# Optimization experiments

Hardware: AMD Instinct MI355X
Metric: run time of the kernel (lower is better)

Reference implementation:

```python
import jax, jax.numpy as jnp
import numpy as np

N_BINS = 15
B, S, V = 2048, 3, 32000

def setup_inputs() -> dict:
    key = jax.random.key(0)
    k1, k2 = jax.random.split(key)
    logits = jax.random.normal(k1, (B, S, V), dtype=jnp.float32)
    targets = jax.random.randint(k2, (B, 4), 0, V, dtype=jnp.int64)
    return {"logits": logits, "targets": targets}

def reference(logits, targets):
    # softmax over vocab, then per-position max confidence and argmax prediction
    probs = jax.nn.softmax(logits, axis=-1)            # [B,S,V]
    p3 = probs[:, :3, :]                               # [B,3,V]
    confidences3 = jnp.max(p3, axis=2)                 # [B,3]
    preds = jnp.argmax(p3, axis=2)                     # [B,3]
    confidences = jnp.prod(confidences3, axis=1)       # [B]
    temp_t = targets[:, 1:]                            # [B,3]
    accuracies = (preds == temp_t).astype(jnp.float32) # [B,3]
    # accuracies[in_bin].mean() over a [n,3] slice == mean of per-row means
    row_acc = jnp.mean(accuracies, axis=1)             # [B]

    boundaries = jnp.linspace(0.0, 1.0, N_BINS + 1)
    lowers, uppers = boundaries[:-1], boundaries[1:]
    # vectorized binning instead of the original per-bin python loop
    in_bin = (confidences[None, :] > lowers[:, None]) & (confidences[None, :] <= uppers[:, None])  # [15,B]
    in_bin_f = in_bin.astype(jnp.float32)
    count = jnp.sum(in_bin_f, axis=1)                  # [15]
    n = jnp.float32(confidences.shape[0])
    prop_in_bin = count / n
    safe_count = jnp.maximum(count, 1.0)
    avg_conf = jnp.sum(in_bin_f * confidences[None, :], axis=1) / safe_count
    avg_acc = jnp.sum(in_bin_f * row_acc[None, :], axis=1) / safe_count
    per_bin = jnp.where(count > 0, jnp.abs(avg_conf - avg_acc) * prop_in_bin, 0.0)
    ece = jnp.sum(per_bin).reshape(1)
    return ece
```

## Files before the change

kernel.cpp:

```cpp
#include <hip/hip_runtime.h>
#include <hip/hip_bf16.h>
#include <math.h>

#define VOCAB   32000
#define BATCH   2048
#define SEQ     3
#define ROWS    (BATCH * SEQ)
#define THREADS 320
#define CHUNK   5
#define NCHUNK  5
#define NBINS   15

__device__ __forceinline__ void combine(float& m, float& s, int& idx,
                                        float m2, float s2, int idx2) {
    if (m2 > m)      { s = s * __expf(m - m2) + s2; m = m2; idx = idx2; }
    else if (m2 < m) { s = s + s2 * __expf(m2 - m); }
    else             { s += s2; idx = (idx2 < idx) ? idx2 : idx; }
}

__global__ __launch_bounds__(THREADS) void row_softmax_stats(
        const float* __restrict__ logits,
        float* __restrict__ maxprob,
        int*   __restrict__ amax)
{
    const int row = blockIdx.x;
    const int t   = threadIdx.x;
    const float4* base = (const float4*)(logits + (size_t)row * VOCAB);

    float m = -INFINITY;
    float s0 = 0.f, s1 = 0.f, s2 = 0.f, s3 = 0.f;
    int   idx = 0;

    float4 cur[CHUNK], nxt[CHUNK];
    #pragma unroll
    for (int u = 0; u < CHUNK; ++u) cur[u] = base[t + THREADS * u];

    #pragma unroll
    for (int c = 0; c < NCHUNK; ++c) {
        if (c + 1 < NCHUNK) {
            #pragma unroll
            for (int u = 0; u < CHUNK; ++u)
                nxt[u] = base[t + THREADS * ((c + 1) * CHUNK + u)];
        }
        #pragma unroll
        for (int u = 0; u < CHUNK; ++u) {
            float4 v = cur[u];
            float lm = fmaxf(fmaxf(v.x, v.y), fmaxf(v.z, v.w));
            if (lm > m) {
                float sc = __expf(m - lm);
                s0 *= sc; s1 *= sc; s2 *= sc; s3 *= sc;
                m = lm;
                const int f4 = t + THREADS * (c * CHUNK + u);
                idx = f4 * 4 + ((v.x == lm) ? 0 : (v.y == lm) ? 1 : (v.z == lm) ? 2 : 3);
            }
            s0 += __expf(v.x - m);
            s1 += __expf(v.y - m);
            s2 += __expf(v.z - m);
            s3 += __expf(v.w - m);
        }
        #pragma unroll
        for (int u = 0; u < CHUNK; ++u) cur[u] = nxt[u];
    }

    float s = (s0 + s1) + (s2 + s3);

    for (int off = 32; off > 0; off >>= 1) {
        float m2 = __shfl_down(m, off);
        float sx = __shfl_down(s, off);
        int   i2 = __shfl_down(idx, off);
        combine(m, s, idx, m2, sx, i2);
    }

    __shared__ float sm[THREADS / 64], ss[THREADS / 64];
    __shared__ int   si[THREADS / 64];
    const int wave = t >> 6;
    if ((t & 63) == 0) { sm[wave] = m; ss[wave] = s; si[wave] = idx; }
    __syncthreads();
    if (t == 0) {
        for (int w = 1; w < THREADS / 64; ++w) combine(m, s, idx, sm[w], ss[w], si[w]);
        maxprob[row] = 1.0f / s;
        amax[row]    = idx;
    }
}

__global__ __launch_bounds__(1024) void ece_reduce(
        const float* __restrict__ maxprob,
        const int*   __restrict__ amax,
        const int*   __restrict__ targets,
        float*       __restrict__ out)
{
    const int t = threadIdx.x;

    float c_cnt[NBINS], c_conf[NBINS], c_acc[NBINS];
    #pragma unroll
    for (int i = 0; i < NBINS; ++i) { c_cnt[i] = 0.f; c_conf[i] = 0.f; c_acc[i] = 0.f; }

    #pragma unroll
    for (int r = 0; r < BATCH / 1024; ++r) {
        const int b = t + r * 1024;
        float p0 = maxprob[b * 3 + 0];
        float p1 = maxprob[b * 3 + 1];
        float p2 = maxprob[b * 3 + 2];
        float conf = (p0 * p1) * p2;

        float acc = 0.f;
        acc += (amax[b * 3 + 0] == targets[b * 4 + 1]) ? 1.f : 0.f;
        acc += (amax[b * 3 + 1] == targets[b * 4 + 2]) ? 1.f : 0.f;
        acc += (amax[b * 3 + 2] == targets[b * 4 + 3]) ? 1.f : 0.f;
        float row_acc = acc * (1.0f / 3.0f);

        #pragma unroll
        for (int i = 0; i < NBINS; ++i) {
            float lo = (float)i       * (1.0f / 15.0f);
            float up = (float)(i + 1) * (1.0f / 15.0f);
            bool in = (conf > lo) && (conf <= up);
            if (in) { c_cnt[i] += 1.f; c_conf[i] += conf; c_acc[i] += row_acc; }
        }
    }

    #pragma unroll
    for (int i = 0; i < NBINS; ++i) {
        for (int off = 32; off > 0; off >>= 1) {
            c_cnt[i]  += __shfl_down(c_cnt[i],  off);
            c_conf[i] += __shfl_down(c_conf[i], off);
            c_acc[i]  += __shfl_down(c_acc[i],  off);
        }
    }

    __shared__ float s_cnt[NBINS], s_conf[NBINS], s_acc[NBINS];
    if (t < NBINS) { s_cnt[t] = 0.f; s_conf[t] = 0.f; s_acc[t] = 0.f; }
    __syncthreads();
    if ((t & 63) == 0) {
        #pragma unroll
        for (int i = 0; i < NBINS; ++i) {
            atomicAdd(&s_cnt[i],  c_cnt[i]);
            atomicAdd(&s_conf[i], c_conf[i]);
            atomicAdd(&s_acc[i],  c_acc[i]);
        }
    }
    __syncthreads();
    if (t == 0) {
        float ece = 0.f;
        #pragma unroll
        for (int i = 0; i < NBINS; ++i) {
            float cnt = s_cnt[i];
            if (cnt > 0.f) {
                float prop     = cnt / (float)BATCH;
                float safe_cnt = fmaxf(cnt, 1.0f);
                float avg_conf = s_conf[i] / safe_cnt;
                float avg_acc  = s_acc[i]  / safe_cnt;
                ece += fabsf(avg_conf - avg_acc) * prop;
            }
        }
        out[0] = ece;
    }
}

extern "C" void kernel_launch(void* const* d_in, const int* in_sizes, int n_in,
                              void* d_out, int out_size, void* d_ws, size_t ws_size,
                              hipStream_t stream) {
    const float* logits  = (const float*)d_in[0];
    const int*   targets = (const int*)d_in[1];
    float*       out     = (float*)d_out;

    float* maxprob = (float*)d_ws;
    int*   amax    = (int*)((char*)d_ws + ROWS * sizeof(float));

    row_softmax_stats<<<ROWS, THREADS, 0, stream>>>(logits, maxprob, amax);
    ece_reduce<<<1, 1024, 0, stream>>>(maxprob, amax, targets, out);
}
```

Measured before the change: 156.1 us.

## Assign one wave per softmax row, drop block reduction, use nontemporal loads

The row-stats kernel now maps each 32000-wide row to a single 64-lane wave, with four rows per 256-thread block, instead of one 320-thread block per row. This removes the shared-memory cross-wave combine and the __syncthreads. Loads become nontemporal vector loads in a simple loop unrolled by 5, replacing the explicit double-buffered prefetch. Each lane now processes 125 float4s serially, which lengthens per-wave dependency chains and relies on occupancy rather than explicit prefetch to hide memory latency.

Measured after the change: 138.3 us. -11.4%, faster.

```diff
diff --git a/kernel.cpp b/kernel.cpp
--- a/kernel.cpp
+++ b/kernel.cpp
@@ -2,14 +2,16 @@
 #include <hip/hip_bf16.h>
 #include <math.h>
 
-#define VOCAB   32000
-#define BATCH   2048
-#define SEQ     3
-#define ROWS    (BATCH * SEQ)
-#define THREADS 320
-#define CHUNK   5
-#define NCHUNK  5
-#define NBINS   15
+#define VOCAB     32000
+#define BATCH     2048
+#define SEQ       3
+#define ROWS      (BATCH * SEQ)
+#define WPB       4
+#define BLOCKSZ   (WPB * 64)
+#define NF4       (VOCAB / 4 / 64)
+#define NBINS     15
+
+typedef float f32x4 __attribute__((ext_vector_type(4)));
 
 __device__ __forceinline__ void combine(float& m, float& s, int& idx,
                                         float m2, float s2, int idx2) {
@@ -18,48 +20,35 @@
     else             { s += s2; idx = (idx2 < idx) ? idx2 : idx; }
 }
 
-__global__ __launch_bounds__(THREADS) void row_softmax_stats(
+__global__ __launch_bounds__(BLOCKSZ) void row_softmax_stats(
         const float* __restrict__ logits,
         float* __restrict__ maxprob,
         int*   __restrict__ amax)
 {
-    const int row = blockIdx.x;
-    const int t   = threadIdx.x;
-    const float4* base = (const float4*)(logits + (size_t)row * VOCAB);
+    const int wave = threadIdx.x >> 6;
+    const int lane = threadIdx.x & 63;
+    const int row  = blockIdx.x * WPB + wave;
+    const f32x4* base = (const f32x4*)(logits + (size_t)row * VOCAB);
 
     float m = -INFINITY;
     float s0 = 0.f, s1 = 0.f, s2 = 0.f, s3 = 0.f;
     int   idx = 0;
 
-    float4 cur[CHUNK], nxt[CHUNK];
-    #pragma unroll
-    for (int u = 0; u < CHUNK; ++u) cur[u] = base[t + THREADS * u];
-
-    #pragma unroll
-    for (int c = 0; c < NCHUNK; ++c) {
-        if (c + 1 < NCHUNK) {
-            #pragma unroll
-            for (int u = 0; u < CHUNK; ++u)
-                nxt[u] = base[t + THREADS * ((c + 1) * CHUNK + u)];
+    #pragma unroll 5
+    for (int i = 0; i < NF4; ++i) {
+        const int f4 = lane + 64 * i;
+        f32x4 v = __builtin_nontemporal_load(base + f4);
+        float lm = fmaxf(fmaxf(v.x, v.y), fmaxf(v.z, v.w));
+        if (lm > m) {
+            float sc = __expf(m - lm);
+            s0 *= sc; s1 *= sc; s2 *= sc; s3 *= sc;
+            m = lm;
+            idx = f4 * 4 + ((v.x == lm) ? 0 : (v.y == lm) ? 1 : (v.z == lm) ? 2 : 3);
         }
-        #pragma unroll
-        for (int u = 0; u < CHUNK; ++u) {
-            float4 v = cur[u];
-            float lm = fmaxf(fmaxf(v.x, v.y), fmaxf(v.z, v.w));
-            if (lm > m) {
-                float sc = __expf(m - lm);
-                s0 *= sc; s1 *= sc; s2 *= sc; s3 *= sc;
-                m = lm;
-                const int f4 = t + THREADS * (c * CHUNK + u);
-                idx = f4 * 4 + ((v.x == lm) ? 0 : (v.y == lm) ? 1 : (v.z == lm) ? 2 : 3);
-            }
-            s0 += __expf(v.x - m);
-            s1 += __expf(v.y - m);
-            s2 += __expf(v.z - m);
-            s3 += __expf(v.w - m);
-        }
-        #pragma unroll
-        for (int u = 0; u < CHUNK; ++u) cur[u] = nxt[u];
+        s0 += __expf(v.x - m);
+        s1 += __expf(v.y - m);
+        s2 += __expf(v.z - m);
+        s3 += __expf(v.w - m);
     }
 
     float s = (s0 + s1) + (s2 + s3);
@@ -71,13 +60,7 @@
         combine(m, s, idx, m2, sx, i2);
     }
 
-    __shared__ float sm[THREADS / 64], ss[THREADS / 64];
-    __shared__ int   si[THREADS / 64];
-    const int wave = t >> 6;
-    if ((t & 63) == 0) { sm[wave] = m; ss[wave] = s; si[wave] = idx; }
-    __syncthreads();
-    if (t == 0) {
-        for (int w = 1; w < THREADS / 64; ++w) combine(m, s, idx, sm[w], ss[w], si[w]);
+    if (lane == 0) {
         maxprob[row] = 1.0f / s;
         amax[row]    = idx;
     }
@@ -166,6 +149,6 @@
     float* maxprob = (float*)d_ws;
     int*   amax    = (int*)((char*)d_ws + ROWS * sizeof(float));
 
-    row_softmax_stats<<<ROWS, THREADS, 0, stream>>>(logits, maxprob, amax);
+    row_softmax_stats<<<ROWS / WPB, BLOCKSZ, 0, stream>>>(logits, maxprob, amax);
     ece_reduce<<<1, 1024, 0, stream>>>(maxprob, amax, targets, out);
 }
```
